# Optimization experiments

Hardware: AMD Instinct MI355X
Metric: run time of the kernel (lower is better)

Reference implementation:

```python
import math
import jax, jax.numpy as jnp
import numpy as np

V, D, E, NH, HD, L, FF, RH = 32000, 512, 4, 8, 64, 2, 2048, 256
MPL, MV = 3, 2  # max_path_len, max_visits_per_expert


def _ln(x):
    m = x.mean(-1, keepdims=True)
    v = ((x - m) ** 2).mean(-1, keepdims=True)
    return (x - m) / jnp.sqrt(v + 1e-5)


def _pe(S, d):
    pos = np.arange(S, dtype=np.float32)[:, None]
    div = np.exp(np.arange(0, d, 2, dtype=np.float32) * (-math.log(10000.0) / d))
    pe = np.zeros((S, d), np.float32)
    pe[:, 0::2] = np.sin(pos * div)
    pe[:, 1::2] = np.cos(pos * div)
    return jnp.asarray(pe)[None]  # [1,S,D]


def setup_inputs() -> dict:
    key = jax.random.key(0)
    ks = jax.random.split(key, 24)
    n = lambda k, shp, s=0.02: (jax.random.normal(k, shp, jnp.float32) * s)
    input_ids = jax.random.randint(ks[0], (8, 256), 0, V, dtype=jnp.int32)
    emb = n(ks[1], (V, D)).at[0].set(0.0)  # padding_idx=0
    return {
        "input_ids": input_ids,
        "emb": emb,
        "r_w1": n(ks[2], (RH, D)), "r_b1": jnp.zeros((RH,), jnp.float32),
        "r_w2": n(ks[3], (E + 1, RH)), "r_b2": jnp.zeros((E + 1,), jnp.float32),
        "r_q": jnp.zeros((E + 1,), jnp.float32),
        "in_w": n(ks[4], (E, L, 3 * D, D)), "in_b": jnp.zeros((E, L, 3 * D), jnp.float32),
        "out_w": n(ks[5], (E, L, D, D)), "out_b": jnp.zeros((E, L, D), jnp.float32),
        "gate_w": n(ks[6], (E, L, D, 2 * D)), "gate_b": jnp.zeros((E, L, D), jnp.float32),
        "f_w1": n(ks[7], (E, L, FF, D)), "f_b1": jnp.zeros((E, L, FF), jnp.float32),
        "f_w2": n(ks[8], (E, L, D, FF)), "f_b2": jnp.zeros((E, L, D), jnp.float32),
        "tag": n(ks[9], (E, 1, 1, D), 0.01),
        "lm_w": n(ks[10], (V, D)), "lm_b": jnp.zeros((V,), jnp.float32),
    }


def reference(input_ids, emb, r_w1, r_b1, r_w2, r_b2, r_q,
              in_w, in_b, out_w, out_b, gate_w, gate_b,
              f_w1, f_b1, f_w2, f_b2, tag, lm_w, lm_b):
    B, S = input_ids.shape

    def mha(h, w, b, ow, ob):
        qkv = h @ w.T + b  # [B,S,3D]
        q, k, v = jnp.split(qkv, 3, axis=-1)
        q = q.reshape(B, S, NH, HD); k = k.reshape(B, S, NH, HD); v = v.reshape(B, S, NH, HD)
        att = jax.nn.softmax(jnp.einsum('bqhd,bkhd->bhqk', q, k) / math.sqrt(HD), axis=-1)
        o = jnp.einsum('bhqk,bkhd->bqhd', att, v).reshape(B, S, D)
        return o @ ow.T + ob

    def expert_fwd(p, h):
        iw, ib, ow, ob, gw, gb, w1, b1, w2, b2, tg = p
        for l in range(L):
            z = _ln(h)  # norm1
            ao = mha(z, iw[l], ib[l], ow[l], ob[l])
            g = jax.nn.sigmoid(jnp.concatenate([z, ao], -1) @ gw[l].T + gb[l])
            h = h + _ln(z + g * ao)  # GatedAttention norm + residual
            z2 = _ln(h)  # norm2
            h = h + jax.nn.gelu(z2 @ w1[l].T + b1[l], approximate=False) @ w2[l].T + b2[l]
        return h + tg

    x = emb[input_ids] * math.sqrt(D)
    x = _ln(x + _pe(S, D))  # pos_encoder + input_norm (dropout=eval identity)

    visits = jnp.zeros((B, E), jnp.int32)
    active = jnp.ones((B,), bool)
    ep = (in_w, in_b, out_w, out_b, gate_w, gate_b, f_w1, f_b1, f_w2, f_b2, tag)

    for _ in range(MPL):
        summary = x.mean(axis=1)  # [B,D]
        logits = jax.nn.gelu(summary @ r_w1.T + r_b1, approximate=False) @ r_w2.T + r_b2
        fl = jnp.clip(_ln(logits + r_q[None, :]), -10.0, 10.0)
        ext = jnp.concatenate([visits >= MV, jnp.zeros((B, 1), bool)], axis=-1)
        fl = jnp.where(ext, -jnp.inf, fl)
        action = jnp.argmax(fl, axis=-1)  # E == terminate
        do = active & (action < E)
        all_out = jax.vmap(expert_fwd, in_axes=(0, None))(ep, x)  # [E,B,S,D]
        sel = jax.nn.one_hot(jnp.where(do, action, 0), E, dtype=x.dtype) * do[:, None].astype(x.dtype)
        nx = jnp.einsum('ebsd,be->bsd', all_out, sel)
        x = jnp.where(do[:, None, None], nx, x)
        visits = visits + (sel > 0).astype(jnp.int32)
        active = do

    return _ln(x) @ lm_w.T + lm_b  # final_norm + lm_head  [B,S,V]
```

## Files before the change

kernel.cpp:

```cpp
#include <hip/hip_runtime.h>
#include <hip/hip_bf16.h>
#include <math.h>

#define BB   8
#define SS   256
#define DD   512
#define NHH  8
#define HDD  64
#define EE   4
#define LL   2
#define FFF  2048
#define RHH  256
#define VV   32000
#define MVV  2
#define TOK  (BB*SS)
#define CASTBLK 44672

typedef __attribute__((ext_vector_type(8))) short bf16x8;
typedef __attribute__((ext_vector_type(4))) float f32x4;

__device__ __forceinline__ float wred_sum(float v){
#pragma unroll
  for(int o=32;o;o>>=1) v += __shfl_xor(v,o,64);
  return v;
}
__device__ __forceinline__ float block_sum(float v, float* sh){
  v = wred_sum(v);
  if((threadIdx.x&63)==0) sh[threadIdx.x>>6]=v;
  __syncthreads();
  float t = sh[0]+sh[1]+sh[2]+sh[3];
  __syncthreads();
  return t;
}
__device__ __forceinline__ float gelu_exact(float x){
  return 0.5f*x*(1.f+erff(x*0.70710678118654752f));
}
__device__ __forceinline__ unsigned short bfr(float f){
  union{float f; unsigned u;} c; c.f=f;
  unsigned u = c.u;
  return (unsigned short)((u + 0x7FFFu + ((u>>16)&1u)) >> 16);
}
__device__ __forceinline__ float bff(unsigned short u){
  union{unsigned u; float f;} c; c.u = ((unsigned)u)<<16; return c.f;
}

__global__ void k_preproc(const float* __restrict__ s0,const float* __restrict__ s1,
                          const float* __restrict__ s2,const float* __restrict__ s3,
                          const float* __restrict__ s4,const float* __restrict__ s5,
                          unsigned short* __restrict__ d0,unsigned short* __restrict__ d1,
                          unsigned short* __restrict__ d2,unsigned short* __restrict__ d3,
                          unsigned short* __restrict__ d4,unsigned short* __restrict__ d5,
                          const int* __restrict__ ids, const float* __restrict__ emb,
                          float* __restrict__ x){
  __shared__ float sh[4];
  if(blockIdx.x < CASTBLK){
    long i = (long)blockIdx.x*256 + threadIdx.x;
    const float* s; unsigned short* d; long o;
    if(i < 1572864L){ s=s0; d=d0; o=i; }
    else if(i < 2097152L){ s=s1; d=d1; o=i-1572864L; }
    else if(i < 3145728L){ s=s2; d=d2; o=i-2097152L; }
    else if(i < 5242880L){ s=s3; d=d3; o=i-3145728L; }
    else if(i < 7340032L){ s=s4; d=d4; o=i-5242880L; }
    else { s=s5; d=d5; o=i-7340032L; }
    float4 v = ((const float4*)s)[o];
    ushort4 u; u.x=bfr(v.x); u.y=bfr(v.y); u.z=bfr(v.z); u.w=bfr(v.w);
    ((ushort4*)d)[o] = u;
    return;
  }
  int tok = blockIdx.x - CASTBLK;
  int s = tok & (SS-1);
  int tid = threadIdx.x;
  int id = ids[tok];
  float v[2];
#pragma unroll
  for(int i=0;i<2;i++){
    int d = tid + i*256;
    float e = emb[(size_t)id*DD + d] * 22.627416997969522f;
    int j = d >> 1;
    float freq = expf((float)(2*j) * (-0.0179889460390160f));
    float arg = (float)s * freq;
    v[i] = e + ((d & 1) ? cosf(arg) : sinf(arg));
  }
  float m = block_sum(v[0]+v[1], sh) * (1.f/DD);
  float dd0=v[0]-m, dd1=v[1]-m;
  float var = block_sum(dd0*dd0+dd1*dd1, sh) * (1.f/DD);
  float inv = rsqrtf(var + 1e-5f);
  float* q = x + (size_t)tok*DD;
  q[tid] = dd0*inv; q[tid+256] = dd1*inv;
}

__global__ __launch_bounds__(256)
void k_compose(const unsigned short* __restrict__ out_wb, const float* __restrict__ out_b,
               const unsigned short* __restrict__ gate_wb,
               unsigned short* __restrict__ wext, float* __restrict__ cb){
  int combo = blockIdx.x;
  const unsigned short* Wa2 = gate_wb + (size_t)combo*DD*2*DD + 512;
  const unsigned short* Wo  = out_wb  + (size_t)combo*DD*DD;
  int c0 = blockIdx.y*64;
  int t = threadIdx.x;
  if(blockIdx.z == 4){
    const float* ob = out_b + (size_t)combo*DD;
    int c = c0 + (t>>2), q = t&3;
    float s = 0.f;
    for(int j=q*128; j<q*128+128; j++) s += bff(Wa2[(size_t)c*1024 + j]) * ob[j];
    s += __shfl_xor(s,1,64);
    s += __shfl_xor(s,2,64);
    if(q==0) cb[(size_t)combo*DD + c] = s;
    return;
  }
  int kb = blockIdx.z*128;
  __shared__ unsigned short sA[64*64];
  __shared__ unsigned short sWT[128*64];
  int lane = t & 63, w = t >> 6;
  int wcol0 = w*32;
  f32x4 acc[4][2];
#pragma unroll
  for(int m=0;m<4;m++)
#pragma unroll
    for(int n=0;n<2;n++) acc[m][n] = (f32x4){0.f,0.f,0.f,0.f};

  for(int j0 = 0; j0 < DD; j0 += 64){
    {
      int sr = t>>3, ss8 = t&7;
#pragma unroll
      for(int i=0;i<2;i++){
        int r = i*32 + sr;
        int ce = ((ss8<<4) ^ ((r&7)<<4)) >> 1;
        const unsigned short* gp = Wa2 + (size_t)(c0+r)*1024 + j0 + ce;
        __builtin_amdgcn_global_load_lds((const __attribute__((address_space(1))) void*)gp,
            (__attribute__((address_space(3))) void*)(sA + i*2048 + t*8), 16, 0, 0);
      }
    }
    {
      int jr = t>>2, cg = (t&3)*32;
      const unsigned short* gp = Wo + (size_t)(j0+jr)*DD + kb + cg;
      bf16x8 v0 = *(const bf16x8*)gp;
      bf16x8 v1 = *(const bf16x8*)(gp+8);
      bf16x8 v2 = *(const bf16x8*)(gp+16);
      bf16x8 v3 = *(const bf16x8*)(gp+24);
#pragma unroll
      for(int e=0;e<8;e++){
        int n0 = cg+e;
        *(unsigned short*)((char*)sWT + n0*128      + ((jr*2) ^ ((n0&7)<<4)))     = (unsigned short)v0[e];
        int n1 = cg+8+e;
        *(unsigned short*)((char*)sWT + n1*128      + ((jr*2) ^ ((n1&7)<<4)))     = (unsigned short)v1[e];
        int n2 = cg+16+e;
        *(unsigned short*)((char*)sWT + n2*128      + ((jr*2) ^ ((n2&7)<<4)))     = (unsigned short)v2[e];
        int n3 = cg+24+e;
        *(unsigned short*)((char*)sWT + n3*128      + ((jr*2) ^ ((n3&7)<<4)))     = (unsigned short)v3[e];
      }
    }
    asm volatile("s_waitcnt vmcnt(0)" ::: "memory");
    __syncthreads();
#pragma unroll
    for(int ks=0; ks<2; ks++){
      bf16x8 af[4], wf[2];
#pragma unroll
      for(int m=0;m<4;m++){
        int r = m*16 + (lane & 15);
        af[m] = *(const bf16x8*)((const char*)sA + r*128 + (((((lane>>4)<<4)|(ks<<6))) ^ ((r&7)<<4)));
      }
#pragma unroll
      for(int n=0;n<2;n++){
        int r = wcol0 + n*16 + (lane & 15);
        wf[n] = *(const bf16x8*)((const char*)sWT + r*128 + (((((lane>>4)<<4)|(ks<<6))) ^ ((r&7)<<4)));
      }
#pragma unroll
      for(int m=0;m<4;m++)
#pragma unroll
        for(int n=0;n<2;n++)
          acc[m][n] = __builtin_amdgcn_mfma_f32_16x16x32_bf16(af[m], wf[n], acc[m][n], 0, 0, 0);
    }
    __syncthreads();
  }
  int orow0 = c0 + ((lane >> 4) << 2);
  int ocol0 = kb + wcol0 + (lane & 15);
#pragma unroll
  for(int m=0;m<4;m++)
#pragma unroll
    for(int n=0;n<2;n++){
      int col = ocol0 + n*16;
#pragma unroll
      for(int j=0;j<4;j++){
        int row = orow0 + m*16 + j;
        wext[(size_t)combo*DD*DD + (size_t)row*DD + col] = bfr(acc[m][n][j]);
      }
    }
}

__global__ void k_lnpsum(const float* __restrict__ xin, const float* __restrict__ P0,
                         const float* __restrict__ P1, float* __restrict__ xout,
                         unsigned short* __restrict__ zb,
                         float* __restrict__ psum, const int* __restrict__ dof){
  __shared__ float sh[4];
  int tid = threadIdx.x;
  if(blockIdx.x < TOK){
    int tok = blockIdx.x; int b = tok>>8;
    size_t base = (size_t)tok*DD;
    float a0 = xin[base+tid], a1 = xin[base+tid+256];
    if(P0){
      if(dof[b]){
        a0 += P0[base+tid]     + P1[base+tid];
        a1 += P0[base+tid+256] + P1[base+tid+256];
      }
      xout[base+tid] = a0; xout[base+tid+256] = a1;
    }
    float m = block_sum(a0+a1, sh) * (1.f/DD);
    float d0=a0-m, d1=a1-m;
    float var = block_sum(d0*d0+d1*d1, sh) * (1.f/DD);
    float inv = rsqrtf(var + 1e-5f);
    zb[base+tid] = bfr(d0*inv); zb[base+tid+256] = bfr(d1*inv);
  } else {
    int pb = blockIdx.x - TOK; int b = pb>>4, p = pb&15;
    bool c = (P0 != nullptr) && dof[b];
    float s0=0.f, s1=0.f;
    for(int tt=0; tt<16; tt++){
      size_t r = (size_t)(b*SS + p*16 + tt)*DD;
      float v0 = xin[r+tid], v1 = xin[r+tid+256];
      if(c){ v0 += P0[r+tid]+P1[r+tid]; v1 += P0[r+tid+256]+P1[r+tid+256]; }
      s0 += v0; s1 += v1;
    }
    float* q = psum + (size_t)(b*16+p)*DD;
    q[tid] = s0; q[tid+256] = s1;
  }
}

__global__ void k_router(const float* __restrict__ psum,
                         const float* __restrict__ r_w1, const float* __restrict__ r_b1,
                         const float* __restrict__ r_w2, const float* __restrict__ r_b2,
                         const float* __restrict__ r_q,
                         int* __restrict__ action, int* __restrict__ dof,
                         int* __restrict__ visits, int* __restrict__ active, int step){
  int b = blockIdx.x; int tid = threadIdx.x;
  if(step==0 && tid==0){ active[b]=1; for(int e=0;e<EE;e++) visits[b*EE+e]=0; }
  __shared__ float ssum[DD];
  __shared__ float hid[RHH];
  __shared__ float lg[EE+1];
  float s0=0.f, s1=0.f;
  for(int p=0;p<16;p++){
    const float* q = psum + (size_t)(b*16+p)*DD;
    s0 += q[tid]; s1 += q[tid+256];
  }
  ssum[tid] = s0*(1.f/SS); ssum[tid+256] = s1*(1.f/SS);
  __syncthreads();
  float acc = r_b1[tid];
  const float4* wr4 = (const float4*)(r_w1 + (size_t)tid*DD);
  for(int d4=0; d4<DD/4; d4++){
    float4 wv = wr4[d4];
    float4 sv = *(const float4*)&ssum[d4*4];
    acc += wv.x*sv.x + wv.y*sv.y + wv.z*sv.z + wv.w*sv.w;
  }
  hid[tid] = gelu_exact(acc);
  __syncthreads();
  if(tid < EE+1){
    const float* w2 = r_w2 + (size_t)tid*RHH;
    float a = r_b2[tid] + r_q[tid];
    for(int j=0;j<RHH;j++) a += hid[j]*w2[j];
    lg[tid]=a;
  }
  __syncthreads();
  if(tid==0){
    float m=0.f; for(int k=0;k<EE+1;k++) m+=lg[k]; m *= (1.f/(EE+1));
    float v=0.f; for(int k=0;k<EE+1;k++){float d=lg[k]-m; v+=d*d;} v *= (1.f/(EE+1));
    float inv = rsqrtf(v+1e-5f);
    float best=-1e38f; int bi=0;
    for(int k=0;k<EE+1;k++){
      float fl = (lg[k]-m)*inv;
      fl = fminf(fmaxf(fl,-10.f),10.f);
      if(k<EE && visits[b*EE+k]>=MVV) fl = -1e38f;
      if(fl > best){best=fl; bi=k;}
    }
    int dd = (active[b] && bi<EE) ? 1 : 0;
    action[b]=bi; dof[b]=dd;
    if(dd) visits[b*EE+bi]++;
    active[b]=dd;
  }
}

template<int EPI>
__device__ __forceinline__ void mg64(
    unsigned short* sA, unsigned short* sW,
    const unsigned short* __restrict__ A, int Ald,
    const unsigned short* __restrict__ W, int Wld,
    const float* __restrict__ bias, const float* __restrict__ tagv,
    int N, int K,
    float* __restrict__ Cf, unsigned short* __restrict__ Cb,
    int rowbase, int colbase){
  int t = threadIdx.x;
  int lane = t & 63;
  int w = t >> 6;
  int wcol0 = w*32;
  int sr = t >> 3, ss8 = t & 7;

  f32x4 acc[4][2];
#pragma unroll
  for(int m=0;m<4;m++)
#pragma unroll
    for(int n=0;n<2;n++) acc[m][n] = (f32x4){0.f,0.f,0.f,0.f};

  auto STAGE = [&](int buf, int k0){
    unsigned short* dA = sA + buf*4096;
    unsigned short* dW = sW + buf*8192;
#pragma unroll
    for(int i = 0; i < 2; i++){
      int r  = i*32 + sr;
      int ce = ((ss8<<4) ^ ((r&7)<<4)) >> 1;
      const unsigned short* gp = A + (size_t)(rowbase + r)*Ald + k0 + ce;
      __builtin_amdgcn_global_load_lds((const __attribute__((address_space(1))) void*)gp,
          (__attribute__((address_space(3))) void*)(dA + i*2048 + t*8), 16, 0, 0);
    }
#pragma unroll
    for(int i = 0; i < 4; i++){
      int r  = i*32 + sr;
      int ce = ((ss8<<4) ^ ((r&7)<<4)) >> 1;
      const unsigned short* gw = W + (size_t)(colbase + r)*Wld + k0 + ce;
      __builtin_amdgcn_global_load_lds((const __attribute__((address_space(1))) void*)gw,
          (__attribute__((address_space(3))) void*)(dW + i*2048 + t*8), 16, 0, 0);
    }
  };

  STAGE(0, 0);
  int cur = 0;
  for(int k0 = 0; k0 < K; k0 += 64){
    if(k0 + 64 < K){
      STAGE(cur^1, k0+64);
      asm volatile("s_waitcnt vmcnt(6)" ::: "memory");
    } else {
      asm volatile("s_waitcnt vmcnt(0)" ::: "memory");
    }
    __builtin_amdgcn_s_barrier();
    __builtin_amdgcn_sched_barrier(0);
    const char* bA = (const char*)(sA + cur*4096);
    const char* bW = (const char*)(sW + cur*8192);
#pragma unroll
    for(int ks = 0; ks < 2; ks++){
      bf16x8 af[4], wf[2];
#pragma unroll
      for(int m = 0; m < 4; m++){
        int r = m*16 + (lane & 15);
        af[m] = *(const bf16x8*)(bA + r*128 + (((((lane>>4)<<4)|(ks<<6))) ^ ((r&7)<<4)));
      }
#pragma unroll
      for(int n = 0; n < 2; n++){
        int r = wcol0 + n*16 + (lane & 15);
        wf[n] = *(const bf16x8*)(bW + r*128 + (((((lane>>4)<<4)|(ks<<6))) ^ ((r&7)<<4)));
      }
#pragma unroll
      for(int m = 0; m < 4; m++)
#pragma unroll
        for(int n = 0; n < 2; n++)
          acc[m][n] = __builtin_amdgcn_mfma_f32_16x16x32_bf16(af[m], wf[n], acc[m][n], 0, 0, 0);
    }
    asm volatile("s_waitcnt lgkmcnt(0)" ::: "memory");
    __builtin_amdgcn_s_barrier();
    cur ^= 1;
  }
  int orow0 = rowbase + ((lane >> 4) << 2);
  int ocol0 = colbase + wcol0 + (lane & 15);
#pragma unroll
  for(int m = 0; m < 4; m++){
#pragma unroll
    for(int n = 0; n < 2; n++){
      int col = ocol0 + n*16;
      float addv = (bias ? bias[col] : 0.f) + (tagv ? tagv[col] : 0.f);
#pragma unroll
      for(int j = 0; j < 4; j++){
        int row = orow0 + m*16 + j;
        size_t idx = (size_t)row*N + col;
        float v = acc[m][n][j] + addv;
        if(EPI == 0){ if(Cf) Cf[idx] = v; if(Cb) Cb[idx] = bfr(v); }
        else if(EPI == 1){ Cb[idx] = bfr(gelu_exact(v)); }
        else { Cf[idx] += v; }
      }
    }
  }
}

#define GEMM_LDS __shared__ unsigned short sA[2*64*64]; __shared__ unsigned short sW[2*128*64];

__global__ __launch_bounds__(256)
void k_qkvgate(const unsigned short* __restrict__ z_bf,
               const unsigned short* __restrict__ in_wb, const float* __restrict__ in_b,
               const unsigned short* __restrict__ gate_wb, const float* __restrict__ gate_b,
               unsigned short* __restrict__ qkv_bf, float* __restrict__ gtmp, int l,
               const int* __restrict__ action, const int* __restrict__ dof){
  GEMM_LDS
  int b = blockIdx.x; if(!dof[b]) return;
  size_t o = (size_t)(action[b]*LL + l);
  int rowbase = b*SS + blockIdx.y*64;
  int zz = blockIdx.z;
  if(zz < 12){
    mg64<0>(sA,sW, z_bf,DD, in_wb + o*3*DD*DD, DD, in_b + o*3*DD, nullptr,
            3*DD, DD, nullptr, qkv_bf, rowbase, zz*128);
  } else {
    mg64<0>(sA,sW, z_bf,DD, gate_wb + o*DD*2*DD, 2*DD, gate_b + o*DD, nullptr,
            DD, DD, gtmp, nullptr, rowbase, (zz-12)*128);
  }
}

__global__ __launch_bounds__(256)
void k_outgate(const unsigned short* __restrict__ attno_bf,
               const unsigned short* __restrict__ out_wb, const float* __restrict__ out_b,
               const unsigned short* __restrict__ wext, const float* __restrict__ cb,
               unsigned short* __restrict__ ao_bf, float* __restrict__ gtmp, int l,
               const int* __restrict__ action, const int* __restrict__ dof){
  GEMM_LDS
  int b = blockIdx.x; if(!dof[b]) return;
  size_t o = (size_t)(action[b]*LL + l);
  int rowbase = b*SS + blockIdx.y*64;
  int zz = blockIdx.z;
  if(zz < 4){
    mg64<0>(sA,sW, attno_bf,DD, out_wb + o*DD*DD, DD, out_b + o*DD, nullptr,
            DD, DD, nullptr, ao_bf, rowbase, zz*128);
  } else {
    mg64<2>(sA,sW, attno_bf,DD, wext + o*DD*DD, DD, cb + o*DD, nullptr,
            DD, DD, gtmp, nullptr, rowbase, (zz-4)*128);
  }
}

__global__ __launch_bounds__(256)
void k_ffn1(const unsigned short* __restrict__ z2_bf,
            const unsigned short* __restrict__ f_w1b, const float* __restrict__ f_b1,
            unsigned short* __restrict__ ffh_bf, int l,
            const int* __restrict__ action, const int* __restrict__ dof){
  GEMM_LDS
  int b = blockIdx.x; if(!dof[b]) return;
  size_t o = (size_t)(action[b]*LL + l);
  mg64<1>(sA,sW, z2_bf,DD, f_w1b + o*FFF*DD, DD, f_b1 + o*FFF, nullptr,
          FFF, DD, nullptr, ffh_bf, b*SS + blockIdx.y*64, blockIdx.z*128);
}

__global__ __launch_bounds__(256)
void k_ffn2(const unsigned short* __restrict__ ffh_bf,
            const unsigned short* __restrict__ f_w2b, const float* __restrict__ f_b2,
            const float* __restrict__ tag,
            float* __restrict__ P0, float* __restrict__ P1, int l,
            const int* __restrict__ action, const int* __restrict__ dof){
  GEMM_LDS
  int b = blockIdx.x; if(!dof[b]) return;
  size_t o = (size_t)(action[b]*LL + l);
  int half = blockIdx.z >> 2, colb = (blockIdx.z & 3)*128;
  const float* bias = half ? nullptr : (f_b2 + o*DD);
  const float* tagv = (half==0 && l==LL-1) ? (tag + (size_t)action[b]*DD) : nullptr;
  mg64<0>(sA,sW, ffh_bf + half*1024, FFF, f_w2b + o*DD*FFF + half*1024, FFF,
          bias, tagv, DD, 1024, half ? P1 : P0, nullptr,
          b*SS + blockIdx.y*64, colb);
}

__global__ __launch_bounds__(256)
void k_attn(const unsigned short* __restrict__ qkv, unsigned short* __restrict__ attno,
            const int* __restrict__ dof){
  int bh = blockIdx.x; int b = bh>>3, h = bh&7;
  if(!dof[b]) return;
  int q0 = blockIdx.y*64;
  __shared__ unsigned short sK[256*64];
  __shared__ unsigned short sVT[64*256];
  int t = threadIdx.x, l = t&63, w = t>>6;
  const unsigned short* qbase = qkv + (size_t)b*SS*1536;

  {
    int sr = t>>3, s8 = t&7;
#pragma unroll
    for(int i=0;i<8;i++){
      int r = i*32 + sr;
      int ce = ((s8<<4) ^ ((r&7)<<4)) >> 1;
      const unsigned short* gp = qbase + (size_t)r*1536 + 512 + h*64 + ce;
      __builtin_amdgcn_global_load_lds((const __attribute__((address_space(1))) void*)gp,
          (__attribute__((address_space(3))) void*)(sK + i*2048 + t*8), 16, 0, 0);
    }
  }
  {
    int kt0 = t>>2, dg = (t&3)*16;
#pragma unroll
    for(int i=0;i<4;i++){
      int kt = i*64 + kt0;
      const unsigned short* gp = qbase + (size_t)kt*1536 + 1024 + h*64 + dg;
      bf16x8 v0 = *(const bf16x8*)gp;
      bf16x8 v1 = *(const bf16x8*)(gp+8);
#pragma unroll
      for(int e=0;e<8;e++){
        int d  = dg+e;
        *(unsigned short*)((char*)sVT + d*512  + ((kt*2) ^ ((d&7)<<4)))  = (unsigned short)v0[e];
        int d2 = dg+8+e;
        *(unsigned short*)((char*)sVT + d2*512 + ((kt*2) ^ ((d2&7)<<4))) = (unsigned short)v1[e];
      }
    }
  }
  bf16x8 qf[2];
  {
    const unsigned short* qrow = qbase + (size_t)(q0 + w*16 + (l&15))*1536 + h*64;
    qf[0] = *(const bf16x8*)(qrow + ((l>>4)<<3));
    qf[1] = *(const bf16x8*)(qrow + ((l>>4)<<3) + 32);
  }
  __syncthreads();

  f32x4 sacc[16];
#pragma unroll
  for(int kb=0;kb<16;kb++) sacc[kb] = (f32x4){0.f,0.f,0.f,0.f};
#pragma unroll
  for(int kb=0;kb<16;kb++){
    int rk = kb*16 + (l&15);
#pragma unroll
    for(int ks=0;ks<2;ks++){
      bf16x8 kf = *(const bf16x8*)((const char*)sK + rk*128 + (((((l>>4)<<4)|(ks<<6))) ^ ((rk&7)<<4)));
      sacc[kb] = __builtin_amdgcn_mfma_f32_16x16x32_bf16(qf[ks], kf, sacc[kb], 0, 0, 0);
    }
  }
  float rden[4];
#pragma unroll
  for(int j=0;j<4;j++){
    float m = -1e38f;
#pragma unroll
    for(int kb=0;kb<16;kb++) m = fmaxf(m, sacc[kb][j]);
#pragma unroll
    for(int o=1;o<16;o<<=1) m = fmaxf(m, __shfl_xor(m,o,64));
    m *= 0.125f;
    float s = 0.f;
#pragma unroll
    for(int kb=0;kb<16;kb++){
      float e = expf(sacc[kb][j]*0.125f - m);
      sacc[kb][j] = e; s += e;
    }
#pragma unroll
    for(int o=1;o<16;o<<=1) s += __shfl_xor(s,o,64);
    rden[j] = 1.f/s;
  }
  __syncthreads();

  char* sP = (char*)sK + w*8192;
#pragma unroll
  for(int kb=0;kb<16;kb++){
    int k = kb*16 + (l&15);
#pragma unroll
    for(int j=0;j<4;j++){
      int qr = ((l>>4)<<2) + j;
      *(unsigned short*)(sP + qr*512 + ((k*2) ^ ((qr&7)<<4))) = bfr(sacc[kb][j]);
    }
  }
  __syncthreads();

  f32x4 oacc[4];
#pragma unroll
  for(int df=0;df<4;df++) oacc[df] = (f32x4){0.f,0.f,0.f,0.f};
#pragma unroll
  for(int kstep=0;kstep<8;kstep++){
    bf16x8 pa = *(const bf16x8*)(sP + (l&15)*512 + ((((kstep<<6)|((l>>4)<<4))) ^ ((l&7)<<4)));
#pragma unroll
    for(int df=0;df<4;df++){
      int d = df*16 + (l&15);
      bf16x8 vb = *(const bf16x8*)((char*)sVT + d*512 + ((((kstep<<6)|((l>>4)<<4))) ^ ((d&7)<<4)));
      oacc[df] = __builtin_amdgcn_mfma_f32_16x16x32_bf16(pa, vb, oacc[df], 0, 0, 0);
    }
  }
  int orow0 = b*SS + q0 + w*16 + ((l>>4)<<2);
#pragma unroll
  for(int df=0;df<4;df++){
    int col = h*64 + df*16 + (l&15);
#pragma unroll
    for(int j=0;j<4;j++)
      attno[(size_t)(orow0+j)*DD + col] = bfr(oacc[df][j]*rden[j]);
  }
}

__global__ void k_gateres_ln(const unsigned short* __restrict__ zb,
                             const unsigned short* __restrict__ aob,
                             const float* __restrict__ g, float* __restrict__ x,
                             unsigned short* __restrict__ z2b, const int* __restrict__ dof){
  int tok = blockIdx.x; if(!dof[tok>>8]) return;
  __shared__ float sh[4];
  int tid=threadIdx.x;
  size_t base=(size_t)tok*DD;
  float zz0=bff(zb[base+tid]),     aa0=bff(aob[base+tid]),     gg0=g[base+tid];
  float zz1=bff(zb[base+tid+256]), aa1=bff(aob[base+tid+256]), gg1=g[base+tid+256];
  float t0 = zz0 + aa0/(1.f+expf(-gg0));
  float t1 = zz1 + aa1/(1.f+expf(-gg1));
  float m = block_sum(t0+t1,sh)*(1.f/DD);
  float d0=t0-m, d1=t1-m;
  float var=block_sum(d0*d0+d1*d1,sh)*(1.f/DD);
  float inv=rsqrtf(var+1e-5f);
  float xn0 = x[base+tid]     + d0*inv;
  float xn1 = x[base+tid+256] + d1*inv;
  x[base+tid] = xn0; x[base+tid+256] = xn1;
  float m2 = block_sum(xn0+xn1,sh)*(1.f/DD);
  float e0=xn0-m2, e1=xn1-m2;
  float var2=block_sum(e0*e0+e1*e1,sh)*(1.f/DD);
  float inv2=rsqrtf(var2+1e-5f);
  z2b[base+tid] = bfr(e0*inv2); z2b[base+tid+256] = bfr(e1*inv2);
}

__global__ __launch_bounds__(512)
void k_lmgemm(const unsigned short* __restrict__ A, const unsigned short* __restrict__ W,
              const float* __restrict__ bias, float* __restrict__ C){
  __shared__ unsigned short sA[2*256*64];
  __shared__ unsigned short sW[2*256*64];
  int t = threadIdx.x, lane = t & 63, w = t >> 6;
  int wr = w >> 2, wc = w & 3;
  int rowbase = blockIdx.y*256, colbase = blockIdx.z*256;
  int sr = t >> 3, ss8 = t & 7;

  f32x4 acc[8][4];
#pragma unroll
  for(int m=0;m<8;m++)
#pragma unroll
    for(int n=0;n<4;n++) acc[m][n] = (f32x4){0.f,0.f,0.f,0.f};

  auto STAGE = [&](int buf, int k0){
    unsigned short* dA = sA + buf*16384;
    unsigned short* dW = sW + buf*16384;
#pragma unroll
    for(int i = 0; i < 4; i++){
      int r  = i*64 + sr;
      int ce = ((ss8<<4) ^ ((r&7)<<4)) >> 1;
      const unsigned short* gp = A + (size_t)(rowbase + r)*DD + k0 + ce;
      __builtin_amdgcn_global_load_lds((const __attribute__((address_space(1))) void*)gp,
          (__attribute__((address_space(3))) void*)(dA + i*4096 + t*8), 16, 0, 0);
      const unsigned short* gw = W + (size_t)(colbase + r)*DD + k0 + ce;
      __builtin_amdgcn_global_load_lds((const __attribute__((address_space(1))) void*)gw,
          (__attribute__((address_space(3))) void*)(dW + i*4096 + t*8), 16, 0, 0);
    }
  };

  STAGE(0, 0);
  int cur = 0;
  for(int k0 = 0; k0 < DD; k0 += 64){
    if(k0 + 64 < DD){
      STAGE(cur^1, k0+64);
      asm volatile("s_waitcnt vmcnt(8)" ::: "memory");
    } else {
      asm volatile("s_waitcnt vmcnt(0)" ::: "memory");
    }
    __builtin_amdgcn_s_barrier();
    __builtin_amdgcn_sched_barrier(0);
    const char* bA = (const char*)(sA + cur*16384);
    const char* bW = (const char*)(sW + cur*16384);
#pragma unroll
    for(int ks = 0; ks < 2; ks++){
      bf16x8 af[8], wf[4];
#pragma unroll
      for(int m = 0; m < 8; m++){
        int r = wr*128 + m*16 + (lane & 15);
        af[m] = *(const bf16x8*)(bA + r*128 + (((((lane>>4)<<4)|(ks<<6))) ^ ((r&7)<<4)));
      }
#pragma unroll
      for(int n = 0; n < 4; n++){
        int r = wc*64 + n*16 + (lane & 15);
        wf[n] = *(const bf16x8*)(bW + r*128 + (((((lane>>4)<<4)|(ks<<6))) ^ ((r&7)<<4)));
      }
#pragma unroll
      for(int m = 0; m < 8; m++)
#pragma unroll
        for(int n = 0; n < 4; n++)
          acc[m][n] = __builtin_amdgcn_mfma_f32_16x16x32_bf16(af[m], wf[n], acc[m][n], 0, 0, 0);
    }
    asm volatile("s_waitcnt lgkmcnt(0)" ::: "memory");
    __builtin_amdgcn_s_barrier();
    cur ^= 1;
  }
  int orow0 = rowbase + wr*128 + ((lane >> 4) << 2);
  int ocol0 = colbase + wc*64 + (lane & 15);
#pragma unroll
  for(int m = 0; m < 8; m++){
#pragma unroll
    for(int n = 0; n < 4; n++){
      int col = ocol0 + n*16;
      float bv = bias[col];
#pragma unroll
      for(int j = 0; j < 4; j++){
        int row = orow0 + m*16 + j;
        C[(size_t)row*VV + col] = acc[m][n][j] + bv;
      }
    }
  }
}

extern "C" void kernel_launch(void* const* d_in, const int* in_sizes, int n_in,
                              void* d_out, int out_size, void* d_ws, size_t ws_size,
                              hipStream_t stream){
  const int*   ids   = (const int*)d_in[0];
  const float* emb   = (const float*)d_in[1];
  const float* r_w1  = (const float*)d_in[2];
  const float* r_b1  = (const float*)d_in[3];
  const float* r_w2  = (const float*)d_in[4];
  const float* r_b2  = (const float*)d_in[5];
  const float* r_q   = (const float*)d_in[6];
  const float* in_w  = (const float*)d_in[7];
  const float* in_b  = (const float*)d_in[8];
  const float* out_w = (const float*)d_in[9];
  const float* out_b = (const float*)d_in[10];
  const float* gate_w= (const float*)d_in[11];
  const float* gate_b= (const float*)d_in[12];
  const float* f_w1  = (const float*)d_in[13];
  const float* f_b1  = (const float*)d_in[14];
  const float* f_w2  = (const float*)d_in[15];
  const float* f_b2  = (const float*)d_in[16];
  const float* tag   = (const float*)d_in[17];
  const float* lm_w  = (const float*)d_in[18];
  const float* lm_b  = (const float*)d_in[19];
  float* out = (float*)d_out;
  float* ws  = (float*)d_ws;

  const size_t M = (size_t)TOK*DD;
  float* x0     = ws;
  float* x1     = ws + 1*M;
  float* gtmp   = ws + 2*M;
  float* P0     = ws + 3*M;
  float* P1     = ws + 4*M;
  float* psum   = ws + 5*M;
  float* cbias  = ws + 5*M + 65536;
  int*   ipool  = (int*)(ws + 5*M + 65536 + 4096);
  int* action = ipool; int* dof = ipool+BB; int* active = ipool+2*BB; int* visits = ipool+3*BB;

  unsigned short* ub = (unsigned short*)(ws + 5*M + 65536 + 4096 + 64);
  unsigned short* z_bf     = ub;
  unsigned short* z2_bf    = ub + 1*M;
  unsigned short* attno_bf = ub + 2*M;
  unsigned short* ao_bf    = ub + 3*M;
  unsigned short* qkv_bf   = ub + 4*M;
  unsigned short* ffh_bf   = ub + 7*M;
  unsigned short* wb = ub + 11*M;
  unsigned short* in_wb   = wb;
  unsigned short* out_wb  = in_wb  + (size_t)EE*LL*3*DD*DD;
  unsigned short* gate_wb = out_wb + (size_t)EE*LL*DD*DD;
  unsigned short* f_w1b   = gate_wb+ (size_t)EE*LL*DD*2*DD;
  unsigned short* f_w2b   = f_w1b  + (size_t)EE*LL*FFF*DD;
  unsigned short* lm_wb   = f_w2b  + (size_t)EE*LL*DD*FFF;
  unsigned short* wext_b  = lm_wb  + (size_t)VV*DD;

  k_preproc<<<CASTBLK+TOK,256,0,stream>>>(in_w,out_w,gate_w,f_w1,f_w2,lm_w,
                                          in_wb,out_wb,gate_wb,f_w1b,f_w2b,lm_wb,
                                          ids, emb, x0);
  k_compose<<<dim3(8,8,5),256,0,stream>>>(out_wb, out_b, gate_wb, wext_b, cbias);

  float* xc = x0;
  for(int step=0; step<3; step++){
    float* xn = (xc==x0) ? x1 : x0;
    if(step==0)
      k_lnpsum<<<TOK+128,256,0,stream>>>(xc, nullptr, nullptr, xn, z_bf, psum, dof);
    else{
      k_lnpsum<<<TOK+128,256,0,stream>>>(xc, P0, P1, xn, z_bf, psum, dof);
      xc = xn;
    }
    k_router<<<BB,256,0,stream>>>(psum,r_w1,r_b1,r_w2,r_b2,r_q,action,dof,visits,active,step);
    for(int l=0; l<LL; l++){
      if(l==1){
        float* xn2 = (xc==x0) ? x1 : x0;
        k_lnpsum<<<TOK,256,0,stream>>>(xc, P0, P1, xn2, z_bf, nullptr, dof);
        xc = xn2;
      }
      k_qkvgate<<<dim3(BB,4,16),256,0,stream>>>(z_bf, in_wb,in_b, gate_wb,gate_b,
                                                qkv_bf, gtmp, l, action, dof);
      k_attn<<<dim3(BB*NHH,4),256,0,stream>>>(qkv_bf, attno_bf, dof);
      k_outgate<<<dim3(BB,4,8),256,0,stream>>>(attno_bf, out_wb,out_b, wext_b,cbias,
                                               ao_bf, gtmp, l, action, dof);
      k_gateres_ln<<<TOK,256,0,stream>>>(z_bf, ao_bf, gtmp, xc, z2_bf, dof);
      k_ffn1<<<dim3(BB,4,16),256,0,stream>>>(z2_bf, f_w1b,f_b1, ffh_bf, l, action, dof);
      k_ffn2<<<dim3(BB,4,8),256,0,stream>>>(ffh_bf, f_w2b,f_b2, tag, P0, P1, l, action, dof);
    }
  }

  {
    float* xn = (xc==x0) ? x1 : x0;
    k_lnpsum<<<TOK,256,0,stream>>>(xc, P0, P1, xn, z_bf, nullptr, dof);
  }
  k_lmgemm<<<dim3(1,8,VV/256),512,0,stream>>>(z_bf, lm_wb, lm_b, out);
}
```

Baseline: 730.7 us.

## Fuse router into LN/psum kernel via last-block atomic; triple-buffer GEMM stages

The router kernel is merged into k_lnpsum. The last of the 16 partial-sum blocks for each batch row, found with an atomic counter, runs the router MLP and argmax inline, which removes three launches. The dof flag is double-buffered so the fused router can write the new flag while other blocks still read the previous one. Separately, the shared GEMM mainloop moves from two-stage to three-stage LDS buffering with deeper vmcnt waits, to overlap more global loads with MFMA. This raises LDS use per block, which may lower occupancy.

```diff
diff --git a/kernel.cpp b/kernel.cpp
--- a/kernel.cpp
+++ b/kernel.cpp
@@ -51,8 +51,9 @@
                           unsigned short* __restrict__ d2,unsigned short* __restrict__ d3,
                           unsigned short* __restrict__ d4,unsigned short* __restrict__ d5,
                           const int* __restrict__ ids, const float* __restrict__ emb,
-                          float* __restrict__ x){
+                          float* __restrict__ x, unsigned* __restrict__ cnt){
   __shared__ float sh[4];
+  if(blockIdx.x==0 && threadIdx.x<8) cnt[threadIdx.x] = 0u;
   if(blockIdx.x < CASTBLK){
     long i = (long)blockIdx.x*256 + threadIdx.x;
     const float* s; unsigned short* d; long o;
@@ -141,13 +142,13 @@
 #pragma unroll
       for(int e=0;e<8;e++){
         int n0 = cg+e;
-        *(unsigned short*)((char*)sWT + n0*128      + ((jr*2) ^ ((n0&7)<<4)))     = (unsigned short)v0[e];
+        *(unsigned short*)((char*)sWT + n0*128 + ((jr*2) ^ ((n0&7)<<4))) = (unsigned short)v0[e];
         int n1 = cg+8+e;
-        *(unsigned short*)((char*)sWT + n1*128      + ((jr*2) ^ ((n1&7)<<4)))     = (unsigned short)v1[e];
+        *(unsigned short*)((char*)sWT + n1*128 + ((jr*2) ^ ((n1&7)<<4))) = (unsigned short)v1[e];
         int n2 = cg+16+e;
-        *(unsigned short*)((char*)sWT + n2*128      + ((jr*2) ^ ((n2&7)<<4)))     = (unsigned short)v2[e];
+        *(unsigned short*)((char*)sWT + n2*128 + ((jr*2) ^ ((n2&7)<<4))) = (unsigned short)v2[e];
         int n3 = cg+24+e;
-        *(unsigned short*)((char*)sWT + n3*128      + ((jr*2) ^ ((n3&7)<<4)))     = (unsigned short)v3[e];
+        *(unsigned short*)((char*)sWT + n3*128 + ((jr*2) ^ ((n3&7)<<4))) = (unsigned short)v3[e];
       }
     }
     asm volatile("s_waitcnt vmcnt(0)" ::: "memory");
@@ -191,15 +192,25 @@
 __global__ void k_lnpsum(const float* __restrict__ xin, const float* __restrict__ P0,
                          const float* __restrict__ P1, float* __restrict__ xout,
                          unsigned short* __restrict__ zb,
-                         float* __restrict__ psum, const int* __restrict__ dof){
+                         float* __restrict__ psum, const int* __restrict__ dofp,
+                         const float* __restrict__ r_w1, const float* __restrict__ r_b1,
+                         const float* __restrict__ r_w2, const float* __restrict__ r_b2,
+                         const float* __restrict__ r_q,
+                         int* __restrict__ action, int* __restrict__ dofc,
+                         int* __restrict__ visits, int* __restrict__ active,
+                         unsigned* __restrict__ cnt, int step){
   __shared__ float sh[4];
+  __shared__ float ssum[DD];
+  __shared__ float hid[RHH];
+  __shared__ float lg[EE+1];
+  __shared__ unsigned rank;
   int tid = threadIdx.x;
   if(blockIdx.x < TOK){
     int tok = blockIdx.x; int b = tok>>8;
     size_t base = (size_t)tok*DD;
     float a0 = xin[base+tid], a1 = xin[base+tid+256];
     if(P0){
-      if(dof[b]){
+      if(dofp[b]){
         a0 += P0[base+tid]     + P1[base+tid];
         a1 += P0[base+tid+256] + P1[base+tid+256];
       }
@@ -210,38 +221,33 @@
     float var = block_sum(d0*d0+d1*d1, sh) * (1.f/DD);
     float inv = rsqrtf(var + 1e-5f);
     zb[base+tid] = bfr(d0*inv); zb[base+tid+256] = bfr(d1*inv);
-  } else {
-    int pb = blockIdx.x - TOK; int b = pb>>4, p = pb&15;
-    bool c = (P0 != nullptr) && dof[b];
-    float s0=0.f, s1=0.f;
-    for(int tt=0; tt<16; tt++){
-      size_t r = (size_t)(b*SS + p*16 + tt)*DD;
-      float v0 = xin[r+tid], v1 = xin[r+tid+256];
-      if(c){ v0 += P0[r+tid]+P1[r+tid]; v1 += P0[r+tid+256]+P1[r+tid+256]; }
-      s0 += v0; s1 += v1;
-    }
-    float* q = psum + (size_t)(b*16+p)*DD;
-    q[tid] = s0; q[tid+256] = s1;
-  }
-}
-
-__global__ void k_router(const float* __restrict__ psum,
-                         const float* __restrict__ r_w1, const float* __restrict__ r_b1,
-                         const float* __restrict__ r_w2, const float* __restrict__ r_b2,
-                         const float* __restrict__ r_q,
-                         int* __restrict__ action, int* __restrict__ dof,
-                         int* __restrict__ visits, int* __restrict__ active, int step){
-  int b = blockIdx.x; int tid = threadIdx.x;
+    return;
+  }
+  int pb = blockIdx.x - TOK; int b = pb>>4, p = pb&15;
+  bool c = (P0 != nullptr) && dofp[b];
+  float s0=0.f, s1=0.f;
+  for(int tt=0; tt<16; tt++){
+    size_t r = (size_t)(b*SS + p*16 + tt)*DD;
+    float v0 = xin[r+tid], v1 = xin[r+tid+256];
+    if(c){ v0 += P0[r+tid]+P1[r+tid]; v1 += P0[r+tid+256]+P1[r+tid+256]; }
+    s0 += v0; s1 += v1;
+  }
+  float* q = psum + (size_t)(b*16+p)*DD;
+  q[tid] = s0; q[tid+256] = s1;
+  __threadfence();
+  if(tid==0)
+    rank = __hip_atomic_fetch_add(&cnt[b], 1u, __ATOMIC_ACQ_REL, __HIP_MEMORY_SCOPE_AGENT);
+  __syncthreads();
+  if(rank != 15u) return;
+  __threadfence();
+  if(tid==0) __hip_atomic_store(&cnt[b], 0u, __ATOMIC_RELAXED, __HIP_MEMORY_SCOPE_AGENT);
   if(step==0 && tid==0){ active[b]=1; for(int e=0;e<EE;e++) visits[b*EE+e]=0; }
-  __shared__ float ssum[DD];
-  __shared__ float hid[RHH];
-  __shared__ float lg[EE+1];
-  float s0=0.f, s1=0.f;
-  for(int p=0;p<16;p++){
-    const float* q = psum + (size_t)(b*16+p)*DD;
-    s0 += q[tid]; s1 += q[tid+256];
-  }
-  ssum[tid] = s0*(1.f/SS); ssum[tid+256] = s1*(1.f/SS);
+  float t0=0.f, t1=0.f;
+  for(int pp=0; pp<16; pp++){
+    const float* qq = psum + (size_t)(b*16+pp)*DD;
+    t0 += qq[tid]; t1 += qq[tid+256];
+  }
+  ssum[tid] = t0*(1.f/SS); ssum[tid+256] = t1*(1.f/SS);
   __syncthreads();
   float acc = r_b1[tid];
   const float4* wr4 = (const float4*)(r_w1 + (size_t)tid*DD);
@@ -271,7 +277,7 @@
       if(fl > best){best=fl; bi=k;}
     }
     int dd = (active[b] && bi<EE) ? 1 : 0;
-    action[b]=bi; dof[b]=dd;
+    action[b]=bi; dofc[b]=dd;
     if(dd) visits[b*EE+bi]++;
     active[b]=dd;
   }
@@ -319,19 +325,25 @@
     }
   };
 
+  int steps = K >> 6;
   STAGE(0, 0);
-  int cur = 0;
-  for(int k0 = 0; k0 < K; k0 += 64){
-    if(k0 + 64 < K){
-      STAGE(cur^1, k0+64);
+  if(steps > 1) STAGE(1, 64);
+  int rb = 0, wb = 2;
+  for(int i = 0; i < steps; i++){
+    if(i + 2 < steps){
+      STAGE(wb, (i+2)<<6);
+      wb = (wb==2) ? 0 : wb+1;
+      asm volatile("s_waitcnt vmcnt(12)" ::: "memory");
+    } else if(i + 1 < steps){
       asm volatile("s_waitcnt vmcnt(6)" ::: "memory");
     } else {
       asm volatile("s_waitcnt vmcnt(0)" ::: "memory");
     }
     __builtin_amdgcn_s_barrier();
     __builtin_amdgcn_sched_barrier(0);
-    const char* bA = (const char*)(sA + cur*4096);
-    const char* bW = (const char*)(sW + cur*8192);
+    const char* bA = (const char*)(sA + rb*4096);
+    const char* bW = (const char*)(sW + rb*8192);
+    rb = (rb==2) ? 0 : rb+1;
 #pragma unroll
     for(int ks = 0; ks < 2; ks++){
       bf16x8 af[4], wf[2];
@@ -353,7 +365,6 @@
     }
     asm volatile("s_waitcnt lgkmcnt(0)" ::: "memory");
     __builtin_amdgcn_s_barrier();
-    cur ^= 1;
   }
   int orow0 = rowbase + ((lane >> 4) << 2);
   int ocol0 = colbase + wcol0 + (lane & 15);
@@ -376,7 +387,7 @@
   }
 }
 
-#define GEMM_LDS __shared__ unsigned short sA[2*64*64]; __shared__ unsigned short sW[2*128*64];
+#define GEMM_LDS __shared__ unsigned short sA[3*64*64]; __shared__ unsigned short sW[3*128*64];
 
 __global__ __launch_bounds__(256)
 void k_qkvgate(const unsigned short* __restrict__ z_bf,
@@ -708,9 +719,14 @@
   float* psum   = ws + 5*M;
   float* cbias  = ws + 5*M + 65536;
   int*   ipool  = (int*)(ws + 5*M + 65536 + 4096);
-  int* action = ipool; int* dof = ipool+BB; int* active = ipool+2*BB; int* visits = ipool+3*BB;
-
-  unsigned short* ub = (unsigned short*)(ws + 5*M + 65536 + 4096 + 64);
+  int* action = ipool;
+  int* dofA   = ipool + 8;
+  int* dofB   = ipool + 16;
+  int* active = ipool + 24;
+  int* visits = ipool + 32;
+  unsigned* cnt = (unsigned*)(ipool + 64);
+
+  unsigned short* ub = (unsigned short*)(ws + 5*M + 65536 + 4096 + 128);
   unsigned short* z_bf     = ub;
   unsigned short* z2_bf    = ub + 1*M;
   unsigned short* attno_bf = ub + 2*M;
@@ -728,39 +744,49 @@
 
   k_preproc<<<CASTBLK+TOK,256,0,stream>>>(in_w,out_w,gate_w,f_w1,f_w2,lm_w,
                                           in_wb,out_wb,gate_wb,f_w1b,f_w2b,lm_wb,
-                                          ids, emb, x0);
+                                          ids, emb, x0, cnt);
   k_compose<<<dim3(8,8,5),256,0,stream>>>(out_wb, out_b, gate_wb, wext_b, cbias);
 
+  int* dofs[2] = {dofA, dofB};
   float* xc = x0;
   for(int step=0; step<3; step++){
+    int* dofp = dofs[step & 1];
+    int* dofc = dofs[(step+1) & 1];
     float* xn = (xc==x0) ? x1 : x0;
     if(step==0)
-      k_lnpsum<<<TOK+128,256,0,stream>>>(xc, nullptr, nullptr, xn, z_bf, psum, dof);
+      k_lnpsum<<<TOK+128,256,0,stream>>>(xc, nullptr, nullptr, xn, z_bf, psum, dofp,
+                                         r_w1,r_b1,r_w2,r_b2,r_q,
+                                         action, dofc, visits, active, cnt, step);
     else{
-      k_lnpsum<<<TOK+128,256,0,stream>>>(xc, P0, P1, xn, z_bf, psum, dof);
+      k_lnpsum<<<TOK+128,256,0,stream>>>(xc, P0, P1, xn, z_bf, psum, dofp,
+                                         r_w1,r_b1,r_w2,r_b2,r_q,
+                                         action, dofc, visits, active, cnt, step);
       xc = xn;
     }
-    k_router<<<BB,256,0,stream>>>(psum,r_w1,r_b1,r_w2,r_b2,r_q,action,dof,visits,active,step);
     for(int l=0; l<LL; l++){
       if(l==1){
         float* xn2 = (xc==x0) ? x1 : x0;
-        k_lnpsum<<<TOK,256,0,stream>>>(xc, P0, P1, xn2, z_bf, nullptr, dof);
+        k_lnpsum<<<TOK,256,0,stream>>>(xc, P0, P1, xn2, z_bf, nullptr, dofc,
+                                       r_w1,r_b1,r_w2,r_b2,r_q,
+                                       action, dofc, visits, active, cnt, step);
         xc = xn2;
       }
       k_qkvgate<<<dim3(BB,4,16),256,0,stream>>>(z_bf, in_wb,in_b, gate_wb,gate_b,
-                                                qkv_bf, gtmp, l, action, dof);
-      k_attn<<<dim3(BB*NHH,4),256,0,stream>>>(qkv_bf, attno_bf, dof);
+                                                qkv_bf, gtmp, l, action, dofc);
+      k_attn<<<dim3(BB*NHH,4),256,0,stream>>>(qkv_bf, attno_bf, dofc);
       k_outgate<<<dim3(BB,4,8),256,0,stream>>>(attno_bf, out_wb,out_b, wext_b,cbias,
-                                               ao_bf, gtmp, l, action, dof);
-      k_gateres_ln<<<TOK,256,0,stream>>>(z_bf, ao_bf, gtmp, xc, z2_bf, dof);
-      k_ffn1<<<dim3(BB,4,16),256,0,stream>>>(z2_bf, f_w1b,f_b1, ffh_bf, l, action, dof);
-      k_ffn2<<<dim3(BB,4,8),256,0,stream>>>(ffh_bf, f_w2b,f_b2, tag, P0, P1, l, action, dof);
+                                               ao_bf, gtmp, l, action, dofc);
+      k_gateres_ln<<<TOK,256,0,stream>>>(z_bf, ao_bf, gtmp, xc, z2_bf, dofc);
+      k_ffn1<<<dim3(BB,4,16),256,0,stream>>>(z2_bf, f_w1b,f_b1, ffh_bf, l, action, dofc);
+      k_ffn2<<<dim3(BB,4,8),256,0,stream>>>(ffh_bf, f_w2b,f_b2, tag, P0, P1, l, action, dofc);
     }
   }
 
   {
     float* xn = (xc==x0) ? x1 : x0;
-    k_lnpsum<<<TOK,256,0,stream>>>(xc, P0, P1, xn, z_bf, nullptr, dof);
+    k_lnpsum<<<TOK,256,0,stream>>>(xc, P0, P1, xn, z_bf, nullptr, dofs[1],
+                                   r_w1,r_b1,r_w2,r_b2,r_q,
+                                   action, dofs[1], visits, active, cnt, 2);
   }
   k_lmgemm<<<dim3(1,8,VV/256),512,0,stream>>>(z_bf, lm_wb, lm_b, out);
 }
```

After: 816.9 us. 1.12x slower.
